# Kernel tuning notes

Measured on AMD Instinct MI355X. Metric: run time of the kernel, lower is better.

Reference implementation:

```python
import jax, jax.numpy as jnp
import numpy as np

NUM_HEADS = 16
ROPE_BASE = 10000.0

def rotate_half(x):
    h = x.shape[-1] // 2
    return jnp.concatenate([-x[..., h:], x[..., :h]], axis=-1)

def setup_inputs() -> dict:
    key = jax.random.key(0)
    k1, k2, k3, k4 = jax.random.split(key, 4)
    B, T, H = 2, 2048, 1024
    hidden_state = jax.random.normal(k1, (B, T, H), dtype=jnp.float32)
    # right-padding mask: per-batch valid lengths
    lengths = jnp.array([2048, 1536], dtype=jnp.int32)
    attention_mask = (jnp.arange(T, dtype=jnp.int32)[None, :] < lengths[:, None]).astype(jnp.int32)
    s = 1.0 / np.sqrt(H)
    w_qkv = jax.random.normal(k2, (H, 3 * H), dtype=jnp.float32) * s
    b_qkv = jax.random.normal(k3, (3 * H,), dtype=jnp.float32) * 0.01
    w_out = jax.random.normal(k4, (H, H), dtype=jnp.float32) * s
    return {"hidden_state": hidden_state, "attention_mask": attention_mask,
            "w_qkv": w_qkv, "b_qkv": b_qkv, "w_out": w_out}

def reference(hidden_state, attention_mask, w_qkv, b_qkv, w_out):
    B, T, H = hidden_state.shape
    hd = H // NUM_HEADS
    qkv = hidden_state @ w_qkv + b_qkv                      # [B,T,3H]
    qkv = qkv.reshape(B, T, NUM_HEADS, 3 * hd).swapaxes(1, 2)  # [B,h,T,3d]
    q, k, v = qkv[..., :hd], qkv[..., hd:2 * hd], qkv[..., 2 * hd:]
    # rotary embedding (cache computed in fp32, as in torch module)
    inv_freq = 1.0 / (ROPE_BASE ** (jnp.arange(0, hd, 2, dtype=jnp.float32) / hd))
    t = jnp.arange(T, dtype=jnp.float32)
    freqs = jnp.outer(t, inv_freq)                          # [T, hd/2]
    emb = jnp.concatenate([freqs, freqs], axis=-1)          # [T, hd]
    cos = jnp.cos(emb)[None, None]                          # [1,1,T,hd]
    sin = jnp.sin(emb)[None, None]
    q = q * cos + rotate_half(q) * sin
    k = k * cos + rotate_half(k) * sin
    scale = 1.0 / jnp.sqrt(jnp.asarray(hd, dtype=q.dtype))
    scores = jnp.einsum('bhqd,bhkd->bhqk', q, k) * scale    # [B,h,T,T]
    causal = jnp.triu(jnp.ones((T, T), dtype=bool), k=1)    # True = masked (future)
    pad = (attention_mask == 0)[:, None, None, :]           # True = masked (padded key)
    mask = causal[None, None] | pad
    scores = jnp.where(mask, jnp.finfo(scores.dtype).min, scores)
    attn = jax.nn.softmax(scores, axis=-1)
    out = jnp.einsum('bhqk,bhkd->bhqd', attn, v)            # [B,h,T,d]
    out = out.swapaxes(1, 2).reshape(B, T, H)
    return out @ w_out
```

## Files before the change

kernel.cpp:

```cpp
#include <hip/hip_runtime.h>
#include <math.h>

typedef __attribute__((ext_vector_type(8))) short short8;
typedef __attribute__((ext_vector_type(4))) short short4v;
typedef __attribute__((ext_vector_type(4))) float floatx4;

#define T_SEQ 2048
#define NHEADS 16
#define HID 1024

#if __has_builtin(__builtin_amdgcn_mfma_f32_16x16x16bf16_1k)
#define MFMA16(a,b,c) __builtin_amdgcn_mfma_f32_16x16x16bf16_1k(a,b,c,0,0,0)
#elif __has_builtin(__builtin_amdgcn_mfma_f32_16x16x16_bf16)
#define MFMA16(a,b,c) __builtin_amdgcn_mfma_f32_16x16x16_bf16(a,b,c,0,0,0)
#else
#define MFMA16(a,b,c) (c)
#endif

__device__ __forceinline__ ushort f2b(float x){
  union { float f; unsigned u; } c; c.f = x;
  unsigned r = c.u + 0x7fffu + ((c.u >> 16) & 1u);
  return (ushort)(r >> 16);
}

__device__ __forceinline__ floatx4 fzero4(){
  floatx4 v; v[0]=0.f; v[1]=0.f; v[2]=0.f; v[3]=0.f; return v;
}

__device__ __forceinline__ void gl_lds16(const ushort* g, ushort* l){
  __builtin_amdgcn_global_load_lds(
      (const __attribute__((address_space(1))) void*)g,
      (__attribute__((address_space(3))) void*)l, 16, 0, 0);
}


__global__ __launch_bounds__(256) void prep(
    const float* __restrict__ hidden, const float* __restrict__ w_qkv,
    const float* __restrict__ w_out, const int* __restrict__ amask,
    ushort* __restrict__ hO, ushort* __restrict__ wqkvT, ushort* __restrict__ woutT,
    float2* __restrict__ cs, int* __restrict__ Lb)
{
  __shared__ __align__(16) char smem[32 * 33 * 4];
  int blk = blockIdx.x;
  int tid = threadIdx.x;

  if (blk < 4096){
    int i = blk * 256 + tid;
    float4 v = ((const float4*)hidden)[i];
    ushort4 o;
    o.x = f2b(v.x); o.y = f2b(v.y); o.z = f2b(v.z); o.w = f2b(v.w);
    ((ushort4*)hO)[i] = o;
  } else if (blk < 8192){
    const float* in; ushort* out; int R, C, bx, by;
    if (blk < 7168){
      int t = blk - 4096; bx = t % 96; by = t / 96;
      in = w_qkv; out = wqkvT; R = 1024; C = 3072;
    } else {
      int t = blk - 7168; bx = t & 31; by = t >> 5;
      in = w_out; out = woutT; R = 1024; C = 1024;
    }
    float (*tile)[33] = (float(*)[33])smem;
    int c0 = bx * 32, r0 = by * 32;
    int tx = tid & 31, ty = tid >> 5;
    #pragma unroll
    for (int i = 0; i < 4; i++){
      int r = ty + i * 8;
      tile[r][tx] = in[(size_t)(r0 + r) * C + c0 + tx];
    }
    __syncthreads();
    #pragma unroll
    for (int i = 0; i < 4; i++){
      int r = ty + i * 8;
      out[(size_t)(c0 + r) * R + r0 + tx] = f2b(tile[tx][r]);
    }
  } else if (blk < 8448){
    int idx = (blk - 8192) * 256 + tid;
    int t = idx >> 5, i = idx & 31;
    float invf = powf(10000.0f, -(float)i / 32.0f);
    float a = (float)t * invf;
    cs[idx] = make_float2(cosf(a), sinf(a));
  } else {
    int b = blk - 8448;
    int* red = (int*)smem;
    int s = 0;
    for (int i = tid; i < T_SEQ; i += 256) s += amask[b * T_SEQ + i];
    red[tid] = s; __syncthreads();
    for (int o = 128; o > 0; o >>= 1){
      if (tid < o) red[tid] += red[tid + o];
      __syncthreads();
    }
    if (tid == 0) Lb[b] = red[0];
  }
}


__global__ __launch_bounds__(256) void gemm_qkv(
    const ushort* __restrict__ A, const ushort* __restrict__ Bt,
    const float* __restrict__ bias,
    ushort* __restrict__ qO, ushort* __restrict__ kO, ushort* __restrict__ vT,
    const float2* __restrict__ cs)
{
  __shared__ __align__(16) ushort As[2][4096];
  __shared__ __align__(16) ushort Bs[2][4096];
  int tid = threadIdx.x;
  int bm = blockIdx.x, bn = blockIdx.y;
  int wave = tid >> 6, lane = tid & 63;
  int wm = wave >> 1, wn = wave & 1;
  int quad = lane >> 4, l15 = lane & 15;

  int srow0 = wave * 32 + (lane >> 2);
  int scol  = (lane & 3) * 8;
  const ushort* baseA = &A[(size_t)(bm * 128 + srow0) * 1024 + scol];
  const ushort* baseB = &Bt[(size_t)(bn * 128 + srow0) * 1024 + scol];

  floatx4 acc[4][4];
  for (int i = 0; i < 4; i++) for (int j = 0; j < 4; j++) acc[i][j] = fzero4();

  gl_lds16(baseA,             &As[0][wave * 1024]);
  gl_lds16(baseA + 16 * 1024, &As[0][wave * 1024 + 512]);
  gl_lds16(baseB,             &Bs[0][wave * 1024]);
  gl_lds16(baseB + 16 * 1024, &Bs[0][wave * 1024 + 512]);
  __syncthreads();

  for (int kt = 0; kt < 32; ++kt){
    int cur = kt & 1;
    if (kt < 31){
      const ushort* gA = baseA + (kt + 1) * 32;
      const ushort* gB = baseB + (kt + 1) * 32;
      gl_lds16(gA,             &As[cur ^ 1][wave * 1024]);
      gl_lds16(gA + 16 * 1024, &As[cur ^ 1][wave * 1024 + 512]);
      gl_lds16(gB,             &Bs[cur ^ 1][wave * 1024]);
      gl_lds16(gB + 16 * 1024, &Bs[cur ^ 1][wave * 1024 + 512]);
    }
    short8 af[4], bfr[4];
    #pragma unroll
    for (int i = 0; i < 4; i++) af[i]  = *(const short8*)&As[cur][(wm * 64 + i * 16 + l15) * 32 + quad * 8];
    #pragma unroll
    for (int i = 0; i < 4; i++) bfr[i] = *(const short8*)&Bs[cur][(wn * 64 + i * 16 + l15) * 32 + quad * 8];
    #pragma unroll
    for (int mt = 0; mt < 4; mt++)
      #pragma unroll
      for (int nt = 0; nt < 4; nt++)
        acc[mt][nt] = __builtin_amdgcn_mfma_f32_16x16x32_bf16(af[mt], bfr[nt], acc[mt][nt], 0, 0, 0);
    __syncthreads();
  }

  int g = bn * 2 + wn;
  int h = g / 3, comp = g - h * 3;

  if (comp == 2){
    #pragma unroll
    for (int nt = 0; nt < 4; nt++){
      int d = nt * 16 + l15;
      float bv = bias[g * 64 + d];
      #pragma unroll
      for (int mt = 0; mt < 4; mt++){
        int row = bm * 128 + wm * 64 + mt * 16 + quad * 4;
        int t = row & (T_SEQ - 1), b_ = row >> 11;
        ushort4 o;
        o.x = f2b(acc[mt][nt][0] + bv);
        o.y = f2b(acc[mt][nt][1] + bv);
        o.z = f2b(acc[mt][nt][2] + bv);
        o.w = f2b(acc[mt][nt][3] + bv);
        *(ushort4*)&vT[(size_t)((b_ * NHEADS + h) * 64 + d) * T_SEQ + t] = o;
      }
    }
  } else {
    ushort* outP = (comp == 0) ? qO : kO;
    float qs = (comp == 0) ? 0.125f : 1.0f;
    float bv[4], bp[4];
    #pragma unroll
    for (int nt = 0; nt < 4; nt++){
      bv[nt] = bias[g * 64 + nt * 16 + l15];
      bp[nt] = bias[g * 64 + ((nt * 16 + l15) ^ 32)];
    }
    #pragma unroll
    for (int mt = 0; mt < 4; mt++)
      #pragma unroll
      for (int r = 0; r < 4; r++){
        int row = bm * 128 + wm * 64 + mt * 16 + quad * 4 + r;
        int t = row & (T_SEQ - 1), b_ = row >> 11;
        float2 c0 = cs[t * 32 + l15];
        float2 c1 = cs[t * 32 + 16 + l15];
        size_t base = (size_t)((b_ * NHEADS + h) * T_SEQ + t) * 64 + l15;
        #pragma unroll
        for (int nt = 0; nt < 4; nt++){
          float cvv = (nt & 1) ? c1.x : c0.x;
          float svv = (nt & 1) ? c1.y : c0.y;
          float sgn = (nt < 2) ? -1.0f : 1.0f;
          float val = acc[mt][nt][r] + bv[nt];
          float pv  = acc[mt][nt ^ 2][r] + bp[nt];
          outP[base + nt * 16] = f2b((val * cvv + sgn * pv * svv) * qs);
        }
      }
  }
}


__global__ __launch_bounds__(256) void attn(
    const ushort* __restrict__ qB, const ushort* __restrict__ kB,
    const ushort* __restrict__ vTB, const int* __restrict__ Lb,
    ushort* __restrict__ oB)
{
  __shared__ __align__(16) ushort SH[2][8192];
  int tid = threadIdx.x;
  int bh = blockIdx.x;
  int qt = 31 - blockIdx.y;
  int b = bh >> 4, h = bh & 15;
  int wave = tid >> 6, lane = tid & 63;
  int quad = lane >> 4, l15 = lane & 15;
  int q0 = qt * 64;
  int L = Lb[b];

  const ushort* Qb  = qB + (size_t)bh * T_SEQ * 64;
  const ushort* Kb  = kB + (size_t)bh * T_SEQ * 64;
  const ushort* VtB = vTB + (size_t)bh * 64 * T_SEQ;

  int qrow = q0 + wave * 16 + l15;
  short8 qf0 = *(const short8*)&Qb[(size_t)qrow * 64 + quad * 8];
  short8 qf1 = *(const short8*)&Qb[(size_t)qrow * 64 + 32 + quad * 8];

  int lr = lane >> 3, ch = lane & 7;
  int sw = (ch ^ lr) * 8;
  int l7 = l15 & 7;

  float m_i = -1e30f, l_i = 0.f;
  floatx4 oacc[4];
  #pragma unroll
  for (int nt = 0; nt < 4; nt++) oacc[nt] = fzero4();

  int lastkb = qt;
  int lkb2 = (L - 1) >> 6;
  if (lkb2 < lastkb) lastkb = lkb2;

  auto stageKV = [&](int kb, int buf){
    int k0 = kb * 64;
    const ushort* gK = &Kb[(size_t)(k0 + wave * 16 + lr) * 64 + sw];
    gl_lds16(gK,          &SH[buf][(wave * 16) * 64]);
    gl_lds16(gK + 8 * 64, &SH[buf][(wave * 16 + 8) * 64]);
    const ushort* gV = &VtB[(size_t)(wave * 16 + lr) * T_SEQ + k0 + sw];
    gl_lds16(gV,             &SH[buf][4096 + (wave * 16) * 64]);
    gl_lds16(gV + 8 * T_SEQ, &SH[buf][4096 + (wave * 16 + 8) * 64]);
  };

  stageKV(0, 0);
  __syncthreads();

  for (int kb = 0; kb <= lastkb; ++kb){
    int cur = kb & 1;
    if (kb < lastkb) stageKV(kb + 1, cur ^ 1);
    const ushort* Ks = &SH[cur][0];
    const ushort* Vt = &SH[cur][4096];
    int k0 = kb * 64;

    floatx4 sacc[4];
    #pragma unroll
    for (int e = 0; e < 4; e++){
      short8 kf0 = *(const short8*)&Ks[(e * 16 + l15) * 64 + ((quad ^ l7) * 8)];
      short8 kf1 = *(const short8*)&Ks[(e * 16 + l15) * 64 + (((quad | 4) ^ l7) * 8)];
      floatx4 z = fzero4();
      z = __builtin_amdgcn_mfma_f32_16x16x32_bf16(kf0, qf0, z, 0, 0, 0);
      z = __builtin_amdgcn_mfma_f32_16x16x32_bf16(kf1, qf1, z, 0, 0, 0);
      sacc[e] = z;
    }

    float s[4][4];
    bool needm = (kb == qt) || (k0 + 64 > L);
    if (needm){
      #pragma unroll
      for (int e = 0; e < 4; e++)
        #pragma unroll
        for (int r = 0; r < 4; r++){
          int key = k0 + e * 16 + quad * 4 + r;
          s[e][r] = (key <= qrow && key < L) ? sacc[e][r] : -1e30f;
        }
    } else {
      #pragma unroll
      for (int e = 0; e < 4; e++)
        #pragma unroll
        for (int r = 0; r < 4; r++) s[e][r] = sacc[e][r];
    }

    float mx = s[0][0];
    #pragma unroll
    for (int e = 0; e < 4; e++)
      #pragma unroll
      for (int r = 0; r < 4; r++) mx = fmaxf(mx, s[e][r]);
    mx = fmaxf(mx, __shfl_xor(mx, 16));
    mx = fmaxf(mx, __shfl_xor(mx, 32));
    float mnew = fmaxf(m_i, mx);
    float alpha = __expf(m_i - mnew);
    m_i = mnew;
    float sum = 0.f;
    #pragma unroll
    for (int e = 0; e < 4; e++)
      #pragma unroll
      for (int r = 0; r < 4; r++){
        float ev = __expf(s[e][r] - mnew);
        s[e][r] = ev;
        sum += ev;
      }
    sum += __shfl_xor(sum, 16);
    sum += __shfl_xor(sum, 32);
    l_i = l_i * alpha + sum;
    #pragma unroll
    for (int nt = 0; nt < 4; nt++)
      #pragma unroll
      for (int r = 0; r < 4; r++) oacc[nt][r] *= alpha;

    short4v pf[4];
    #pragma unroll
    for (int e = 0; e < 4; e++){
      union { unsigned u[2]; short4v v; } pk;
      pk.u[0] = (__float_as_uint(s[e][1]) & 0xffff0000u) | (__float_as_uint(s[e][0]) >> 16);
      pk.u[1] = (__float_as_uint(s[e][3]) & 0xffff0000u) | (__float_as_uint(s[e][2]) >> 16);
      pf[e] = pk.v;
    }

    #pragma unroll
    for (int nt = 0; nt < 4; nt++){
      #pragma unroll
      for (int e = 0; e < 4; e++){
        int cw = e * 2 + (quad >> 1);
        short4v vf = *(const short4v*)&Vt[(nt * 16 + l15) * 64 + ((cw ^ l7) * 8) + (quad & 1) * 4];
        oacc[nt] = MFMA16(vf, pf[e], oacc[nt]);
      }
    }
    __syncthreads();
  }

  float inv = 1.f / l_i;
  ushort (*Ot)[80] = (ushort(*)[80])&SH[0][0];
  #pragma unroll
  for (int nt = 0; nt < 4; nt++){
    ushort4 o;
    o.x = f2b(oacc[nt][0] * inv);
    o.y = f2b(oacc[nt][1] * inv);
    o.z = f2b(oacc[nt][2] * inv);
    o.w = f2b(oacc[nt][3] * inv);
    *(ushort4*)&Ot[wave * 16 + l15][nt * 16 + quad * 4] = o;
  }
  __syncthreads();
  int r = tid >> 2, c = (tid & 3) * 16;
  short8 o0 = *(const short8*)&Ot[r][c];
  short8 o1 = *(const short8*)&Ot[r][c + 8];
  ushort* dst = &oB[(size_t)((b * T_SEQ + q0 + r) * NHEADS + h) * 64 + c];
  *(short8*)dst = o0;
  *(short8*)(dst + 8) = o1;
}


__global__ __launch_bounds__(256) void gemm_out_k(
    const ushort* __restrict__ A, const ushort* __restrict__ Bt,
    float* __restrict__ out)
{
  __shared__ __align__(16) ushort As[2][4096];
  __shared__ __align__(16) ushort Bs[2][4096];
  int tid = threadIdx.x;
  int bm = blockIdx.x, bn = blockIdx.y;
  int wave = tid >> 6, lane = tid & 63;
  int wm = wave >> 1, wn = wave & 1;
  int quad = lane >> 4, l15 = lane & 15;

  int srow0 = wave * 32 + (lane >> 2);
  int scol  = (lane & 3) * 8;
  const ushort* baseA = &A[(size_t)(bm * 128 + srow0) * 1024 + scol];
  const ushort* baseB = &Bt[(size_t)(bn * 128 + srow0) * 1024 + scol];

  floatx4 acc[4][4];
  for (int i = 0; i < 4; i++) for (int j = 0; j < 4; j++) acc[i][j] = fzero4();

  gl_lds16(baseA,             &As[0][wave * 1024]);
  gl_lds16(baseA + 16 * 1024, &As[0][wave * 1024 + 512]);
  gl_lds16(baseB,             &Bs[0][wave * 1024]);
  gl_lds16(baseB + 16 * 1024, &Bs[0][wave * 1024 + 512]);
  __syncthreads();

  for (int kt = 0; kt < 32; ++kt){
    int cur = kt & 1;
    if (kt < 31){
      const ushort* gA = baseA + (kt + 1) * 32;
      const ushort* gB = baseB + (kt + 1) * 32;
      gl_lds16(gA,             &As[cur ^ 1][wave * 1024]);
      gl_lds16(gA + 16 * 1024, &As[cur ^ 1][wave * 1024 + 512]);
      gl_lds16(gB,             &Bs[cur ^ 1][wave * 1024]);
      gl_lds16(gB + 16 * 1024, &Bs[cur ^ 1][wave * 1024 + 512]);
    }
    short8 af[4], bfr[4];
    #pragma unroll
    for (int i = 0; i < 4; i++) af[i]  = *(const short8*)&As[cur][(wm * 64 + i * 16 + l15) * 32 + quad * 8];
    #pragma unroll
    for (int i = 0; i < 4; i++) bfr[i] = *(const short8*)&Bs[cur][(wn * 64 + i * 16 + l15) * 32 + quad * 8];
    #pragma unroll
    for (int mt = 0; mt < 4; mt++)
      #pragma unroll
      for (int nt = 0; nt < 4; nt++)
        acc[mt][nt] = __builtin_amdgcn_mfma_f32_16x16x32_bf16(af[mt], bfr[nt], acc[mt][nt], 0, 0, 0);
    __syncthreads();
  }

  #pragma unroll
  for (int nt = 0; nt < 4; nt++){
    int n = bn * 128 + wn * 64 + nt * 16 + l15;
    #pragma unroll
    for (int mt = 0; mt < 4; mt++)
      #pragma unroll
      for (int r = 0; r < 4; r++){
        int row = bm * 128 + wm * 64 + mt * 16 + quad * 4 + r;
        out[(size_t)row * 1024 + n] = acc[mt][nt][r];
      }
  }
}


extern "C" void kernel_launch(void* const* d_in, const int* in_sizes, int n_in,
                              void* d_out, int out_size, void* d_ws, size_t ws_size,
                              hipStream_t stream)
{
  const float* hidden = (const float*)d_in[0];
  const int*   amask  = (const int*)d_in[1];
  const float* w_qkv  = (const float*)d_in[2];
  const float* b_qkv  = (const float*)d_in[3];
  const float* w_out  = (const float*)d_in[4];
  float* out = (float*)d_out;

  char* ws = (char*)d_ws;
  ushort* hO    = (ushort*)(ws);
  ushort* wqkvT = (ushort*)(ws + 8388608);
  ushort* woutT = (ushort*)(ws + 14680064);
  ushort* qB    = (ushort*)(ws + 16777216);
  ushort* kB    = (ushort*)(ws + 25165824);
  ushort* vT    = (ushort*)(ws + 33554432);
  float2* cs    = (float2*)(ws + 41943040);
  int*    Lb    = (int*)(ws + 42467328);

  prep<<<8450, 256, 0, stream>>>(hidden, w_qkv, w_out, amask, hO, wqkvT, woutT, cs, Lb);
  gemm_qkv<<<dim3(32, 24), 256, 0, stream>>>(hO, wqkvT, b_qkv, qB, kB, vT, cs);
  attn<<<dim3(32, 32), 256, 0, stream>>>(qB, kB, vT, Lb, hO );
  gemm_out_k<<<dim3(32, 8), 256, 0, stream>>>(hO, woutT, out);
}
```

Before: 195.4 us.

## Pair causal query tiles per attention block, use exp2 softmax, halve out-GEMM tile N

Each attention block now handles two query tiles (p and 31-p), sharing the staged K/V tiles so that causal work per block is balanced and K/V loads are reused. Log2(e) is folded into the Q scale so the softmax can use the hardware exp2. The output GEMM tile width drops from 128 to 64 columns, doubling the grid to 512 blocks for better CU occupancy. The cost is more registers per attention thread (two accumulator sets) and fewer attention blocks (512).

```diff
diff --git a/kernel.cpp b/kernel.cpp
--- a/kernel.cpp
+++ b/kernel.cpp
@@ -15,6 +15,12 @@
 #define MFMA16(a,b,c) __builtin_amdgcn_mfma_f32_16x16x16_bf16(a,b,c,0,0,0)
 #else
 #define MFMA16(a,b,c) (c)
+#endif
+
+#if __has_builtin(__builtin_amdgcn_exp2f)
+#define EXP2F(x) __builtin_amdgcn_exp2f(x)
+#else
+#define EXP2F(x) exp2f(x)
 #endif
 
 __device__ __forceinline__ ushort f2b(float x){
@@ -167,7 +173,7 @@
     }
   } else {
     ushort* outP = (comp == 0) ? qO : kO;
-    float qs = (comp == 0) ? 0.125f : 1.0f;
+    float qs = (comp == 0) ? 0.125f * 1.44269504089f : 1.0f;
     float bv[4], bp[4];
     #pragma unroll
     for (int nt = 0; nt < 4; nt++){
@@ -205,33 +211,36 @@
   __shared__ __align__(16) ushort SH[2][8192];
   int tid = threadIdx.x;
   int bh = blockIdx.x;
-  int qt = 31 - blockIdx.y;
+  int p  = blockIdx.y;
+  int qtA = p, qtB = 31 - p;
   int b = bh >> 4, h = bh & 15;
   int wave = tid >> 6, lane = tid & 63;
   int quad = lane >> 4, l15 = lane & 15;
-  int q0 = qt * 64;
   int L = Lb[b];
 
   const ushort* Qb  = qB + (size_t)bh * T_SEQ * 64;
   const ushort* Kb  = kB + (size_t)bh * T_SEQ * 64;
   const ushort* VtB = vTB + (size_t)bh * 64 * T_SEQ;
 
-  int qrow = q0 + wave * 16 + l15;
-  short8 qf0 = *(const short8*)&Qb[(size_t)qrow * 64 + quad * 8];
-  short8 qf1 = *(const short8*)&Qb[(size_t)qrow * 64 + 32 + quad * 8];
+  int qrowA = qtA * 64 + wave * 16 + l15;
+  int qrowB = qtB * 64 + wave * 16 + l15;
+  short8 qfA0 = *(const short8*)&Qb[(size_t)qrowA * 64 + quad * 8];
+  short8 qfA1 = *(const short8*)&Qb[(size_t)qrowA * 64 + 32 + quad * 8];
+  short8 qfB0 = *(const short8*)&Qb[(size_t)qrowB * 64 + quad * 8];
+  short8 qfB1 = *(const short8*)&Qb[(size_t)qrowB * 64 + 32 + quad * 8];
 
   int lr = lane >> 3, ch = lane & 7;
   int sw = (ch ^ lr) * 8;
   int l7 = l15 & 7;
 
-  float m_i = -1e30f, l_i = 0.f;
-  floatx4 oacc[4];
+  float mA = -1e30f, lA = 0.f, mB = -1e30f, lB = 0.f;
+  floatx4 oA[4], oB4[4];
   #pragma unroll
-  for (int nt = 0; nt < 4; nt++) oacc[nt] = fzero4();
-
-  int lastkb = qt;
-  int lkb2 = (L - 1) >> 6;
-  if (lkb2 < lastkb) lastkb = lkb2;
+  for (int nt = 0; nt < 4; nt++){ oA[nt] = fzero4(); oB4[nt] = fzero4(); }
+
+  int Lcap = (L - 1) >> 6;
+  int lastA = qtA < Lcap ? qtA : Lcap;
+  int lastB = qtB < Lcap ? qtB : Lcap;
 
   auto stageKV = [&](int kb, int buf){
     int k0 = kb * 64;
@@ -246,76 +255,87 @@
   stageKV(0, 0);
   __syncthreads();
 
-  for (int kb = 0; kb <= lastkb; ++kb){
+  for (int kb = 0; kb <= lastB; ++kb){
     int cur = kb & 1;
-    if (kb < lastkb) stageKV(kb + 1, cur ^ 1);
+    if (kb < lastB) stageKV(kb + 1, cur ^ 1);
     const ushort* Ks = &SH[cur][0];
     const ushort* Vt = &SH[cur][4096];
     int k0 = kb * 64;
-
-    floatx4 sacc[4];
+    bool aAct = (kb <= lastA);
+
+    floatx4 sAa[4], sBa[4];
     #pragma unroll
     for (int e = 0; e < 4; e++){
       short8 kf0 = *(const short8*)&Ks[(e * 16 + l15) * 64 + ((quad ^ l7) * 8)];
       short8 kf1 = *(const short8*)&Ks[(e * 16 + l15) * 64 + (((quad | 4) ^ l7) * 8)];
       floatx4 z = fzero4();
-      z = __builtin_amdgcn_mfma_f32_16x16x32_bf16(kf0, qf0, z, 0, 0, 0);
-      z = __builtin_amdgcn_mfma_f32_16x16x32_bf16(kf1, qf1, z, 0, 0, 0);
-      sacc[e] = z;
-    }
-
-    float s[4][4];
-    bool needm = (kb == qt) || (k0 + 64 > L);
-    if (needm){
+      z = __builtin_amdgcn_mfma_f32_16x16x32_bf16(kf0, qfB0, z, 0, 0, 0);
+      z = __builtin_amdgcn_mfma_f32_16x16x32_bf16(kf1, qfB1, z, 0, 0, 0);
+      sBa[e] = z;
+      if (aAct){
+        floatx4 z2 = fzero4();
+        z2 = __builtin_amdgcn_mfma_f32_16x16x32_bf16(kf0, qfA0, z2, 0, 0, 0);
+        z2 = __builtin_amdgcn_mfma_f32_16x16x32_bf16(kf1, qfA1, z2, 0, 0, 0);
+        sAa[e] = z2;
+      }
+    }
+
+    short4v pfA[4], pfB[4];
+    auto softmax_tile = [&](floatx4* sa, float& m_i, float& l_i, floatx4* oacc,
+                            int qrow, int qt, short4v* pf){
+      float s[4][4];
+      bool needm = (kb == qt) || (k0 + 64 > L);
+      if (needm){
+        #pragma unroll
+        for (int e = 0; e < 4; e++)
+          #pragma unroll
+          for (int r = 0; r < 4; r++){
+            int key = k0 + e * 16 + quad * 4 + r;
+            s[e][r] = (key <= qrow && key < L) ? sa[e][r] : -1e30f;
+          }
+      } else {
+        #pragma unroll
+        for (int e = 0; e < 4; e++)
+          #pragma unroll
+          for (int r = 0; r < 4; r++) s[e][r] = sa[e][r];
+      }
+      float mx = s[0][0];
       #pragma unroll
       for (int e = 0; e < 4; e++)
         #pragma unroll
+        for (int r = 0; r < 4; r++) mx = fmaxf(mx, s[e][r]);
+      mx = fmaxf(mx, __shfl_xor(mx, 16));
+      mx = fmaxf(mx, __shfl_xor(mx, 32));
+      float mnew = fmaxf(m_i, mx);
+      float alpha = EXP2F(m_i - mnew);
+      m_i = mnew;
+      float sum = 0.f;
+      #pragma unroll
+      for (int e = 0; e < 4; e++)
+        #pragma unroll
         for (int r = 0; r < 4; r++){
-          int key = k0 + e * 16 + quad * 4 + r;
-          s[e][r] = (key <= qrow && key < L) ? sacc[e][r] : -1e30f;
+          float ev = EXP2F(s[e][r] - mnew);
+          s[e][r] = ev;
+          sum += ev;
         }
-    } else {
-      #pragma unroll
-      for (int e = 0; e < 4; e++)
-        #pragma unroll
-        for (int r = 0; r < 4; r++) s[e][r] = sacc[e][r];
-    }
-
-    float mx = s[0][0];
-    #pragma unroll
-    for (int e = 0; e < 4; e++)
-      #pragma unroll
-      for (int r = 0; r < 4; r++) mx = fmaxf(mx, s[e][r]);
-    mx = fmaxf(mx, __shfl_xor(mx, 16));
-    mx = fmaxf(mx, __shfl_xor(mx, 32));
-    float mnew = fmaxf(m_i, mx);
-    float alpha = __expf(m_i - mnew);
-    m_i = mnew;
-    float sum = 0.f;
-    #pragma unroll
-    for (int e = 0; e < 4; e++)
-      #pragma unroll
-      for (int r = 0; r < 4; r++){
-        float ev = __expf(s[e][r] - mnew);
-        s[e][r] = ev;
-        sum += ev;
-      }
-    sum += __shfl_xor(sum, 16);
-    sum += __shfl_xor(sum, 32);
-    l_i = l_i * alpha + sum;
-    #pragma unroll
-    for (int nt = 0; nt < 4; nt++)
-      #pragma unroll
-      for (int r = 0; r < 4; r++) oacc[nt][r] *= alpha;
-
-    short4v pf[4];
-    #pragma unroll
-    for (int e = 0; e < 4; e++){
-      union { unsigned u[2]; short4v v; } pk;
-      pk.u[0] = (__float_as_uint(s[e][1]) & 0xffff0000u) | (__float_as_uint(s[e][0]) >> 16);
-      pk.u[1] = (__float_as_uint(s[e][3]) & 0xffff0000u) | (__float_as_uint(s[e][2]) >> 16);
-      pf[e] = pk.v;
-    }
+      sum += __shfl_xor(sum, 16);
+      sum += __shfl_xor(sum, 32);
+      l_i = l_i * alpha + sum;
+      #pragma unroll
+      for (int nt = 0; nt < 4; nt++)
+        #pragma unroll
+        for (int r = 0; r < 4; r++) oacc[nt][r] *= alpha;
+      #pragma unroll
+      for (int e = 0; e < 4; e++){
+        union { unsigned u[2]; short4v v; } pk;
+        pk.u[0] = (__float_as_uint(s[e][1]) & 0xffff0000u) | (__float_as_uint(s[e][0]) >> 16);
+        pk.u[1] = (__float_as_uint(s[e][3]) & 0xffff0000u) | (__float_as_uint(s[e][2]) >> 16);
+        pf[e] = pk.v;
+      }
+    };
+
+    softmax_tile(sBa, mB, lB, oB4, qrowB, qtB, pfB);
+    if (aAct) softmax_tile(sAa, mA, lA, oA, qrowA, qtA, pfA);
 
     #pragma unroll
     for (int nt = 0; nt < 4; nt++){
@@ -323,30 +343,42 @@
       for (int e = 0; e < 4; e++){
         int cw = e * 2 + (quad >> 1);
         short4v vf = *(const short4v*)&Vt[(nt * 16 + l15) * 64 + ((cw ^ l7) * 8) + (quad & 1) * 4];
-        oacc[nt] = MFMA16(vf, pf[e], oacc[nt]);
+        oB4[nt] = MFMA16(vf, pfB[e], oB4[nt]);
+        if (aAct) oA[nt] = MFMA16(vf, pfA[e], oA[nt]);
       }
     }
     __syncthreads();
   }
 
-  float inv = 1.f / l_i;
-  ushort (*Ot)[80] = (ushort(*)[80])&SH[0][0];
+  float invA = 1.f / lA, invB = 1.f / lB;
+  ushort (*OtA)[80] = (ushort(*)[80])&SH[0][0];
+  ushort (*OtB)[80] = (ushort(*)[80])&SH[0][5120];
   #pragma unroll
   for (int nt = 0; nt < 4; nt++){
-    ushort4 o;
-    o.x = f2b(oacc[nt][0] * inv);
-    o.y = f2b(oacc[nt][1] * inv);
-    o.z = f2b(oacc[nt][2] * inv);
-    o.w = f2b(oacc[nt][3] * inv);
-    *(ushort4*)&Ot[wave * 16 + l15][nt * 16 + quad * 4] = o;
+    ushort4 oa, ob;
+    oa.x = f2b(oA[nt][0] * invA);  oa.y = f2b(oA[nt][1] * invA);
+    oa.z = f2b(oA[nt][2] * invA);  oa.w = f2b(oA[nt][3] * invA);
+    ob.x = f2b(oB4[nt][0] * invB); ob.y = f2b(oB4[nt][1] * invB);
+    ob.z = f2b(oB4[nt][2] * invB); ob.w = f2b(oB4[nt][3] * invB);
+    *(ushort4*)&OtA[wave * 16 + l15][nt * 16 + quad * 4] = oa;
+    *(ushort4*)&OtB[wave * 16 + l15][nt * 16 + quad * 4] = ob;
   }
   __syncthreads();
   int r = tid >> 2, c = (tid & 3) * 16;
-  short8 o0 = *(const short8*)&Ot[r][c];
-  short8 o1 = *(const short8*)&Ot[r][c + 8];
-  ushort* dst = &oB[(size_t)((b * T_SEQ + q0 + r) * NHEADS + h) * 64 + c];
-  *(short8*)dst = o0;
-  *(short8*)(dst + 8) = o1;
+  {
+    short8 o0 = *(const short8*)&OtA[r][c];
+    short8 o1 = *(const short8*)&OtA[r][c + 8];
+    ushort* dst = &oB[(size_t)((b * T_SEQ + qtA * 64 + r) * NHEADS + h) * 64 + c];
+    *(short8*)dst = o0;
+    *(short8*)(dst + 8) = o1;
+  }
+  {
+    short8 o0 = *(const short8*)&OtB[r][c];
+    short8 o1 = *(const short8*)&OtB[r][c + 8];
+    ushort* dst = &oB[(size_t)((b * T_SEQ + qtB * 64 + r) * NHEADS + h) * 64 + c];
+    *(short8*)dst = o0;
+    *(short8*)(dst + 8) = o1;
+  }
 }
 
 
@@ -355,25 +387,24 @@
     float* __restrict__ out)
 {
   __shared__ __align__(16) ushort As[2][4096];
-  __shared__ __align__(16) ushort Bs[2][4096];
+  __shared__ __align__(16) ushort Bs[2][2048];
   int tid = threadIdx.x;
   int bm = blockIdx.x, bn = blockIdx.y;
   int wave = tid >> 6, lane = tid & 63;
   int wm = wave >> 1, wn = wave & 1;
   int quad = lane >> 4, l15 = lane & 15;
 
-  int srow0 = wave * 32 + (lane >> 2);
-  int scol  = (lane & 3) * 8;
-  const ushort* baseA = &A[(size_t)(bm * 128 + srow0) * 1024 + scol];
-  const ushort* baseB = &Bt[(size_t)(bn * 128 + srow0) * 1024 + scol];
-
-  floatx4 acc[4][4];
-  for (int i = 0; i < 4; i++) for (int j = 0; j < 4; j++) acc[i][j] = fzero4();
+  int lr4 = lane >> 2;
+  int sc  = (lane & 3) * 8;
+  const ushort* baseA = &A[(size_t)(bm * 128 + wave * 32 + lr4) * 1024 + sc];
+  const ushort* baseB = &Bt[(size_t)(bn * 64 + wave * 16 + lr4) * 1024 + sc];
+
+  floatx4 acc[4][2];
+  for (int i = 0; i < 4; i++) for (int j = 0; j < 2; j++) acc[i][j] = fzero4();
 
   gl_lds16(baseA,             &As[0][wave * 1024]);
   gl_lds16(baseA + 16 * 1024, &As[0][wave * 1024 + 512]);
-  gl_lds16(baseB,             &Bs[0][wave * 1024]);
-  gl_lds16(baseB + 16 * 1024, &Bs[0][wave * 1024 + 512]);
+  gl_lds16(baseB,             &Bs[0][wave * 512]);
   __syncthreads();
 
   for (int kt = 0; kt < 32; ++kt){
@@ -383,25 +414,24 @@
       const ushort* gB = baseB + (kt + 1) * 32;
       gl_lds16(gA,             &As[cur ^ 1][wave * 1024]);
       gl_lds16(gA + 16 * 1024, &As[cur ^ 1][wave * 1024 + 512]);
-      gl_lds16(gB,             &Bs[cur ^ 1][wave * 1024]);
-      gl_lds16(gB + 16 * 1024, &Bs[cur ^ 1][wave * 1024 + 512]);
-    }
-    short8 af[4], bfr[4];
+      gl_lds16(gB,             &Bs[cur ^ 1][wave * 512]);
+    }
+    short8 af[4], bfr[2];
     #pragma unroll
     for (int i = 0; i < 4; i++) af[i]  = *(const short8*)&As[cur][(wm * 64 + i * 16 + l15) * 32 + quad * 8];
     #pragma unroll
-    for (int i = 0; i < 4; i++) bfr[i] = *(const short8*)&Bs[cur][(wn * 64 + i * 16 + l15) * 32 + quad * 8];
+    for (int j = 0; j < 2; j++) bfr[j] = *(const short8*)&Bs[cur][(wn * 32 + j * 16 + l15) * 32 + quad * 8];
     #pragma unroll
     for (int mt = 0; mt < 4; mt++)
       #pragma unroll
-      for (int nt = 0; nt < 4; nt++)
+      for (int nt = 0; nt < 2; nt++)
         acc[mt][nt] = __builtin_amdgcn_mfma_f32_16x16x32_bf16(af[mt], bfr[nt], acc[mt][nt], 0, 0, 0);
     __syncthreads();
   }
 
   #pragma unroll
-  for (int nt = 0; nt < 4; nt++){
-    int n = bn * 128 + wn * 64 + nt * 16 + l15;
+  for (int nt = 0; nt < 2; nt++){
+    int n = bn * 64 + wn * 32 + nt * 16 + l15;
     #pragma unroll
     for (int mt = 0; mt < 4; mt++)
       #pragma unroll
@@ -436,6 +466,6 @@
 
   prep<<<8450, 256, 0, stream>>>(hidden, w_qkv, w_out, amask, hO, wqkvT, woutT, cs, Lb);
   gemm_qkv<<<dim3(32, 24), 256, 0, stream>>>(hO, wqkvT, b_qkv, qB, kB, vT, cs);
-  attn<<<dim3(32, 32), 256, 0, stream>>>(qB, kB, vT, Lb, hO );
-  gemm_out_k<<<dim3(32, 8), 256, 0, stream>>>(hO, woutT, out);
-}
+  attn<<<dim3(32, 16), 256, 0, stream>>>(qB, kB, vT, Lb, hO );
+  gemm_out_k<<<dim3(32, 16), 256, 0, stream>>>(hO, woutT, out);
+}
```

After: 198.8 us. About the same (+1.7%).
